# Optimization experiments

Hardware: AMD Instinct MI355X
Metric: run time of the kernel (lower is better)

The kernel has to match this reference:

```python
import jax, jax.numpy as jnp
import numpy as np

ROTARY_BASE = 10000
INFTY_APPROX = 1e30
B, T, M, H, D = 2, 2048, 2048, 16, 128


def rope(x):
    # x: [B, T, H, D]; half-split rotary encoding
    *_, length, _, width = x.shape
    half = width // 2
    positions = jnp.arange(length, dtype=jnp.float32)[None, :, None, None]      # [1,T,1,1]
    dims = jnp.arange(half, dtype=jnp.float32)
    ang_freqs = jnp.power(float(ROTARY_BASE), -dims / half)[None, None, None, :]  # [1,1,1,D/2]
    radians = positions * ang_freqs
    cos = jnp.cos(radians).astype(x.dtype)
    sin = jnp.sin(radians).astype(x.dtype)
    even, odd = x[..., :half], x[..., half:]
    r_even = even * cos - odd * sin
    r_odd = even * sin + odd * cos
    return jnp.concatenate([r_even, r_odd], axis=-1)


def setup_inputs() -> dict:
    key = jax.random.key(0)
    k0, k1, k2, k3, k4 = jax.random.split(key, 5)
    return {
        "x": jax.random.normal(k0, (B, T, M), dtype=jnp.float32),
        "w_aq": jax.random.normal(k1, (H, M, D), dtype=jnp.float32) * (M ** -0.5),
        "w_ak": jax.random.normal(k2, (H, M, D), dtype=jnp.float32) * (M ** -0.5),
        "w_av": jax.random.normal(k3, (H, M, D), dtype=jnp.float32) * (M ** -0.5),
        "w_ao": jax.random.normal(k4, (H, D, M), dtype=jnp.float32) * ((2 * 24 * M) ** -0.5),
    }


def reference(x, w_aq, w_ak, w_av, w_ao):
    q = jnp.einsum("btm,hmd->bthd", x, w_aq)
    k = jnp.einsum("btm,hmd->bthd", x, w_ak)
    v = jnp.einsum("btm,hmd->bthd", x, w_av)
    q = rope(q)
    k = rope(k)
    # muP attention scaling: 1/d_head (not 1/sqrt(d_head))
    mult = (1.0 / D) ** 0.5
    s = jnp.einsum("bihd,bjhd->bhij", mult * q, mult * k)  # [B,H,T,T]
    i = jnp.arange(T)[:, None]
    j = jnp.arange(T)[None, :]
    mask = (i < j)[None, None, :, :]  # mask future positions
    s = s - jnp.asarray(INFTY_APPROX, dtype=x.dtype) * mask
    p = jax.nn.softmax(s, axis=-1)
    o = jnp.einsum("bhij,bjhd->bihd", p, v)
    r = jnp.einsum("bihd,hdm->bim", o, w_ao)
    return r
```

## Files before the change

### kernel.cpp

```cpp
#include <hip/hip_runtime.h>

#define Bb 2
#define Tt 2048
#define Mm 2048
#define Hh 16
#define Dd 128

typedef __attribute__((ext_vector_type(8))) short bf16x8;
typedef __attribute__((ext_vector_type(4))) float f32x4;
typedef __attribute__((ext_vector_type(16))) float f32x16;

__device__ __forceinline__ unsigned short f2bf(float f) {
    unsigned int u = __builtin_bit_cast(unsigned int, f);
    u += 0x7FFFu + ((u >> 16) & 1u);
    return (unsigned short)(u >> 16);
}

__device__ __forceinline__ unsigned int cvt_pk_bf16(float lo, float hi) {
    unsigned int r;
    asm("v_cvt_pk_bf16_f32 %0, %1, %2" : "=v"(r) : "v"(lo), "v"(hi));
    return r;
}

__device__ __forceinline__ float fexp2(float x) { return __builtin_amdgcn_exp2f(x); }

__device__ __forceinline__ void gld16(const void* g, void* l) {
    __builtin_amdgcn_global_load_lds(
        (const __attribute__((address_space(1))) void*)g,
        (__attribute__((address_space(3))) void*)l, 16, 0, 0);
}


__global__ __launch_bounds__(256) void cvt_x2(const float* __restrict__ x,
                                              unsigned short* __restrict__ xb2) {
    const int blk = blockIdx.x;
    const int mt = blk >> 5, kt = blk & 31;
#pragma unroll
    for (int it = 0; it < 4; ++it) {
        int s = it * 256 + threadIdx.x;
        int row = ((s >> 6) & 3) * 32 + (s & 31);
        int k = (s >> 8) * 16 + ((s >> 5) & 1) * 8;
        const float* sp = x + ((long)(mt * 128 + row)) * 2048 + kt * 64 + k;
        float4 a = *(const float4*)sp;
        float4 b = *(const float4*)(sp + 4);
        uint4 pk;
        pk.x = (unsigned int)f2bf(a.x) | ((unsigned int)f2bf(a.y) << 16);
        pk.y = (unsigned int)f2bf(a.z) | ((unsigned int)f2bf(a.w) << 16);
        pk.z = (unsigned int)f2bf(b.x) | ((unsigned int)f2bf(b.y) << 16);
        pk.w = (unsigned int)f2bf(b.z) | ((unsigned int)f2bf(b.w) << 16);
        *(uint4*)(xb2 + (((long)(mt * 32 + kt)) * 1024 + s) * 8) = pk;
    }
}

__global__ __launch_bounds__(256) void w_qkv_tile(
    const float* __restrict__ wq, const float* __restrict__ wk, const float* __restrict__ wv,
    unsigned short* __restrict__ outBase) {
    __shared__ float tile[64][132];
    const int kt = blockIdx.x;
    const int zy = blockIdx.y;
    const int which = zy >> 4, head = zy & 15;
    const float* src = (which == 0 ? wq : which == 1 ? wk : wv) + (long)head * 2048 * 128;
    const int tid = threadIdx.x;
#pragma unroll
    for (int it = 0; it < 8; ++it) {
        int f = it * 256 + tid;
        int row = f >> 5, c4 = f & 31;
        float4 v = *(const float4*)(src + (long)(kt * 64 + row) * 128 + c4 * 4);
        tile[row][c4 * 4 + 0] = v.x;
        tile[row][c4 * 4 + 1] = v.y;
        tile[row][c4 * 4 + 2] = v.z;
        tile[row][c4 * 4 + 3] = v.w;
    }
    __syncthreads();
    unsigned short* outp = outBase + (((long)(which * 16 + head)) * 32 + kt) * 1024 * 8;
#pragma unroll
    for (int it = 0; it < 4; ++it) {
        int up = it * 256 + tid;
        int kk = up >> 8, nf = (up >> 6) & 3, l = up & 63;
        int il = l & 31, hl = l >> 5;
        int d = il + 64 * (nf & 1) + 32 * (nf >> 1);
        int kl = kk * 16 + hl * 8;
        uint4 pk;
        pk.x = (unsigned int)f2bf(tile[kl + 0][d]) | ((unsigned int)f2bf(tile[kl + 1][d]) << 16);
        pk.y = (unsigned int)f2bf(tile[kl + 2][d]) | ((unsigned int)f2bf(tile[kl + 3][d]) << 16);
        pk.z = (unsigned int)f2bf(tile[kl + 4][d]) | ((unsigned int)f2bf(tile[kl + 5][d]) << 16);
        pk.w = (unsigned int)f2bf(tile[kl + 6][d]) | ((unsigned int)f2bf(tile[kl + 7][d]) << 16);
        *(uint4*)(outp + (long)up * 8) = pk;
    }
}

__global__ __launch_bounds__(256) void transpose_cvt(const float* __restrict__ in,
                                                     unsigned short* __restrict__ out,
                                                     int rows, int cols,
                                                     long in_slab, long out_slab) {
    __shared__ float tile[32][33];
    const float* ip = in + (long)blockIdx.z * in_slab;
    unsigned short* op = out + (long)blockIdx.z * out_slab;
    int r0 = blockIdx.x * 32, c0 = blockIdx.y * 32;
    int tx = threadIdx.x & 31, ty = threadIdx.x >> 5;
#pragma unroll
    for (int j = 0; j < 32; j += 8)
        tile[ty + j][tx] = ip[(long)(r0 + ty + j) * cols + c0 + tx];
    __syncthreads();
#pragma unroll
    for (int j = 0; j < 32; j += 8)
        op[(long)(c0 + ty + j) * rows + r0 + tx] = f2bf(tile[tx][ty + j]);
}

__global__ __launch_bounds__(256) void rope_tab(float* __restrict__ cosT,
                                                float* __restrict__ sinT) {
    int idx = blockIdx.x * 256 + threadIdx.x;
    int t = idx >> 6, d = idx & 63;
    float freq = powf(10000.f, -(float)d / 64.f);
    float ang = (float)t * freq;
    sinT[idx] = sinf(ang);
    cosT[idx] = cosf(ang);
}

template <bool WIDE>
__device__ __forceinline__ void proj_sub(
    const unsigned short* __restrict__ xb2,
    const unsigned short* __restrict__ wT2,
    char* lds, int bm, int offc,
    unsigned short* __restrict__ qO, unsigned short* __restrict__ kO,
    unsigned short* __restrict__ vtO,
    const float* __restrict__ cosT, const float* __restrict__ sinT, int tid) {
    const int lane = tid & 63, wave = tid >> 6;
    const int il = lane & 31, hl = lane >> 5;
    const int wm = WIDE ? (wave >> 2) : (wave >> 1);
    const int wn = WIDE ? (wave & 3) : (wave & 1);
    const int hseg0 = offc >> 7;
    const int mode = offc >> 11;
    constexpr int MF = WIDE ? 4 : 2;

    f32x16 acc[MF][2];
#pragma unroll
    for (int a = 0; a < MF; ++a)
#pragma unroll
        for (int b2 = 0; b2 < 2; ++b2)
#pragma unroll
            for (int e = 0; e < 16; ++e) acc[a][b2][e] = 0.f;

    auto stage = [&](int buf, int t, int half) {
        const int kt = t >> 1, hf = t & 1;
        char* dst = lds + buf * 32768;
        if (WIDE) {
#pragma unroll
            for (int i = 0; i < 2; ++i) {
                int f = (half * 2 + i) * 512 + tid;
                if (f < 1024) {
                    int kk = f >> 9, rf = (f >> 6) & 7, l = f & 63;
                    int mt = 2 * bm + (rf >> 2), rb = rf & 3;
                    gld16(xb2 + (((long)(mt * 32 + kt)) * 1024 + (2 * hf + kk) * 256 + rb * 64 + l) * 8,
                          dst + f * 16);
                } else {
                    int g = f - 1024;
                    int kk = g >> 9, cf = (g >> 6) & 7, l = g & 63;
                    int hs = hseg0 + (cf >> 2), nf = cf & 3;
                    gld16(wT2 + (((long)(hs * 32 + kt)) * 1024 + (2 * hf + kk) * 256 + nf * 64 + l) * 8,
                          dst + 16384 + g * 16);
                }
            }
        } else {
            const int i0 = half ? 2 : 0, i1 = half ? 3 : 2;
            for (int i = i0; i < i1; ++i) {
                int f = i * 512 + tid;
                if (f < 1024) {
                    int kk = f >> 9, rf = (f >> 6) & 7, l = f & 63;
                    int mt = 2 * bm + (rf >> 2), rb = rf & 3;
                    gld16(xb2 + (((long)(mt * 32 + kt)) * 1024 + (2 * hf + kk) * 256 + rb * 64 + l) * 8,
                          dst + f * 16);
                } else {
                    int g = f - 1024;
                    int kk = g >> 8, nf = (g >> 6) & 3, l = g & 63;
                    gld16(wT2 + (((long)(hseg0 * 32 + kt)) * 1024 + (2 * hf + kk) * 256 + nf * 64 + l) * 8,
                          dst + 16384 + g * 16);
                }
            }
        }
    };

    stage(0, 0, 0); stage(0, 0, 1);
    stage(1, 1, 0); stage(1, 1, 1);

    int cur = 0;
    for (int t = 0; t < 64; ++t) {
        int pre = cur + 2; if (pre >= 3) pre -= 3;
        const char* bc = lds + cur * 32768;

        if (t + 2 < 64) {
            stage(pre, t + 2, 0);
            if (WIDE) asm volatile("s_waitcnt vmcnt(6)" ::: "memory");
            else      asm volatile("s_waitcnt vmcnt(5)" ::: "memory");
        } else if (t == 62) {
            if (WIDE) asm volatile("s_waitcnt vmcnt(4)" ::: "memory");
            else      asm volatile("s_waitcnt vmcnt(3)" ::: "memory");
        } else {
            asm volatile("s_waitcnt vmcnt(0)" ::: "memory");
        }
        asm volatile("s_barrier" ::: "memory");
        {
            bf16x8 af[MF], bf[2];
#pragma unroll
            for (int mf = 0; mf < MF; ++mf)
                af[mf] = *(const bf16x8*)(bc + ((wm * MF + mf) * 64 + lane) * 16);
#pragma unroll
            for (int nf = 0; nf < 2; ++nf)
                bf[nf] = *(const bf16x8*)(bc + 16384 + ((wn * 2 + nf) * 64 + lane) * 16);
            asm volatile("s_waitcnt lgkmcnt(0)" ::: "memory");
            __builtin_amdgcn_s_setprio(1);
#pragma unroll
            for (int mf = 0; mf < MF; ++mf)
#pragma unroll
                for (int nf = 0; nf < 2; ++nf)
                    acc[mf][nf] = __builtin_amdgcn_mfma_f32_32x32x16_bf16(af[mf], bf[nf], acc[mf][nf], 0, 0, 0);
            __builtin_amdgcn_s_setprio(0);
        }
        asm volatile("s_barrier" ::: "memory");

        if (t + 2 < 64) stage(pre, t + 2, 1);
        asm volatile("s_barrier" ::: "memory");
        {
            constexpr int BO = WIDE ? 512 : 256;
            bf16x8 af[MF], bf[2];
#pragma unroll
            for (int mf = 0; mf < MF; ++mf)
                af[mf] = *(const bf16x8*)(bc + (512 + (wm * MF + mf) * 64 + lane) * 16);
#pragma unroll
            for (int nf = 0; nf < 2; ++nf)
                bf[nf] = *(const bf16x8*)(bc + 16384 + (BO + (wn * 2 + nf) * 64 + lane) * 16);
            asm volatile("s_waitcnt lgkmcnt(0)" ::: "memory");
            __builtin_amdgcn_s_setprio(1);
#pragma unroll
            for (int mf = 0; mf < MF; ++mf)
#pragma unroll
                for (int nf = 0; nf < 2; ++nf)
                    acc[mf][nf] = __builtin_amdgcn_mfma_f32_32x32x16_bf16(af[mf], bf[nf], acc[mf][nf], 0, 0, 0);
            __builtin_amdgcn_s_setprio(0);
        }
        asm volatile("s_barrier" ::: "memory");
        cur = (cur == 2) ? 0 : cur + 1;
    }
    asm volatile("s_waitcnt vmcnt(0)" ::: "memory");
    __syncthreads();

    const int b = bm >> 3;
    const int t0 = (bm & 7) * 256;
    const int head_g = WIDE ? (hseg0 + (wn >> 1)) : hseg0;
    const int head_l = head_g & 15;
    const int opar = WIDE ? (wn & 1) : wn;
    constexpr int WMS = WIDE ? 128 : 64;

    if (mode < 2) {
        const float qs = (mode == 0) ? 0.011271055f : 1.0f;
        unsigned short* outp = (mode == 0) ? qO : kO;
        long hb = ((long)(b * Hh + head_l)) * Tt;
        int d_lo = il + 32 * opar;
#pragma unroll
        for (int mf = 0; mf < MF; ++mf)
#pragma unroll
            for (int reg = 0; reg < 16; ++reg) {
                int r = (reg & 3) + 8 * (reg >> 2) + 4 * hl;
                int tt = t0 + wm * WMS + mf * 32 + r;
                float c = cosT[tt * 64 + d_lo], s = sinT[tt * 64 + d_lo];
                float ev = acc[mf][0][reg], od = acc[mf][1][reg];
                long base = (hb + tt) * Dd;
                outp[base + d_lo]      = f2bf((ev * c - od * s) * qs);
                outp[base + d_lo + 64] = f2bf((ev * s + od * c) * qs);
            }
    } else {
        char* patch = lds + wave * 4096;
        long hdbase = ((long)(b * Hh + head_l)) * Dd * Tt;
#pragma unroll
        for (int mf = 0; mf < MF; ++mf) {
#pragma unroll
            for (int nf = 0; nf < 2; ++nf) {
                int dslot = nf * 32 + il;
                int swz = (dslot & 3) << 4;
#pragma unroll
                for (int qg = 0; qg < 4; ++qg) {
                    uint2 w;
                    w.x = cvt_pk_bf16(acc[mf][nf][qg * 4 + 0], acc[mf][nf][qg * 4 + 1]);
                    w.y = cvt_pk_bf16(acc[mf][nf][qg * 4 + 2], acc[mf][nf][qg * 4 + 3]);
                    *(uint2*)(patch + dslot * 64 + ((qg * 16 + hl * 8) ^ swz)) = w;
                }
            }
            __builtin_amdgcn_s_waitcnt(0);
#pragma unroll
            for (int p = 0; p < 4; ++p) {
                int dslot = p * 16 + (lane >> 2);
                int t8 = lane & 3;
                uint4 v = *(const uint4*)(patch + dslot * 64 + ((t8 * 16) ^ ((dslot & 3) << 4)));
                int o = opar * 2 + (dslot >> 5), il2 = dslot & 31;
                int dd = il2 + 32 * (o >> 1) + 64 * (o & 1);
                int tg = t0 + wm * WMS + mf * 32 + t8 * 8;
                *(uint4*)(vtO + hdbase + (long)dd * Tt + tg) = v;
            }
            __builtin_amdgcn_s_waitcnt(0);
        }
    }
}

__global__ __launch_bounds__(512, 2) void proj_gemm7(
    const unsigned short* __restrict__ xb2,
    const unsigned short* __restrict__ wT2,
    unsigned short* __restrict__ qO,
    unsigned short* __restrict__ kO,
    unsigned short* __restrict__ vtO,
    const float* __restrict__ cosT,
    const float* __restrict__ sinT) {
    __shared__ __align__(16) char lds[98304];
    const int bm = blockIdx.x;
    const int bc = blockIdx.y;
    const int s = bc * 384;
    const bool swap = ((s & 2047) == 1920);
    const int offw = swap ? s + 128 : s;
    const int offn = swap ? s : s + 256;
    const int tid = threadIdx.x;

    proj_sub<true>(xb2, wT2, lds, bm, offw, qO, kO, vtO, cosT, sinT, tid);
    __syncthreads();
    proj_sub<false>(xb2, wT2, lds, bm, offn, qO, kO, vtO, cosT, sinT, tid);
}

__global__ __launch_bounds__(256) void attn_kernel(
    const unsigned short* __restrict__ q,
    const unsigned short* __restrict__ k,
    const unsigned short* __restrict__ vt,
    unsigned short* __restrict__ o) {
    __shared__ __align__(16) unsigned short lds[32768];

    const int lid = (int)blockIdx.x;
    const int p = lid & 255;
    const int bh = p & 31;
    const int q0 = p >> 5;
    const int qb = (lid >> 8) ? (15 - q0) : q0;

    const int tid = threadIdx.x, lane = tid & 63, wave = tid >> 6;
    const int h = lane >> 5, iln = lane & 31;

    const unsigned short* qp = q + (long)bh * Tt * Dd;
    const unsigned short* kp = k + (long)bh * Tt * Dd;
    const unsigned short* vp = vt + (long)bh * Dd * Tt;

    const int i_g = qb * 128 + wave * 32 + iln;
    bf16x8 qf[8];
#pragma unroll
    for (int kk = 0; kk < 8; ++kk)
        qf[kk] = *(const bf16x8*)(qp + (long)i_g * Dd + kk * 16 + h * 8);

    f32x16 accO[4];
#pragma unroll
    for (int nb = 0; nb < 4; ++nb)
#pragma unroll
        for (int e = 0; e < 16; ++e) accO[nb][e] = 0.f;

    float m_r = -1e30f, l_r = 0.f;
    const int ntiles = 2 * qb + 2;

    auto stage = [&](int buf, int tix) {
        const int j0s = tix * 64;
#pragma unroll
        for (int it = 0; it < 4; ++it) {
            int f = it * 256 + tid;
            int rk = f >> 4, ck = f & 15;
            gld16(kp + ((long)(j0s + rk) * Dd + ((ck ^ (rk & 7)) << 3)),
                  (char*)lds + buf * 16384 + f * 16);
            int rv = f >> 3, cv = f & 7;
            gld16(vp + ((long)rv * Tt + j0s + ((cv ^ (rv & 7)) << 3)),
                  (char*)lds + 32768 + buf * 16384 + f * 16);
        }
    };

    stage(0, 0);

    for (int tix = 0; tix < ntiles; ++tix) {
        const int cur = tix & 1;
        const int j0 = tix * 64;
        if (tix + 1 < ntiles) {
            stage(cur ^ 1, tix + 1);
            asm volatile("s_waitcnt vmcnt(8)" ::: "memory");
        } else {
            asm volatile("s_waitcnt vmcnt(0)" ::: "memory");
        }
        __builtin_amdgcn_s_barrier();

        const char* Kb = (const char*)lds + cur * 16384;
        const char* Vb = (const char*)lds + 32768 + cur * 16384;

        f32x16 sacc[2];
#pragma unroll
        for (int mb = 0; mb < 2; ++mb)
#pragma unroll
            for (int e = 0; e < 16; ++e) sacc[mb][e] = 0.f;

        __builtin_amdgcn_s_setprio(1);
#pragma unroll
        for (int mb = 0; mb < 2; ++mb) {
            int row = mb * 32 + iln;
            const char* Kr = Kb + row * 256;
            int sw = row & 7;
#pragma unroll
            for (int kk = 0; kk < 8; ++kk) {
                bf16x8 kf = *(const bf16x8*)(Kr + 16 * ((kk * 2 + h) ^ sw));
                sacc[mb] = __builtin_amdgcn_mfma_f32_32x32x16_bf16(kf, qf[kk], sacc[mb], 0, 0, 0);
            }
        }
        __builtin_amdgcn_s_setprio(0);

        const bool domask = (j0 + 63 > qb * 128);
        if (domask) {
#pragma unroll
            for (int mb = 0; mb < 2; ++mb)
#pragma unroll
                for (int reg = 0; reg < 16; ++reg) {
                    int j = j0 + mb * 32 + (reg & 3) + 8 * (reg >> 2) + 4 * h;
                    if (j > i_g) sacc[mb][reg] = -1e30f;
                }
        }

        float red[16];
#pragma unroll
        for (int r = 0; r < 16; ++r) red[r] = fmaxf(sacc[0][r], sacc[1][r]);
#pragma unroll
        for (int s = 8; s >= 1; s >>= 1)
#pragma unroll
            for (int r = 0; r < s; ++r) red[r] = fmaxf(red[r], red[r + s]);
        float mx = fmaxf(red[0], __shfl_xor(red[0], 32, 64));

        if (__any(mx > m_r + 8.f)) {
            float mn = fmaxf(m_r, mx);
            float corr = fexp2(m_r - mn);
            m_r = mn;
            l_r *= corr;
#pragma unroll
            for (int reg = 0; reg < 16; ++reg) {
                int rrow = (reg & 3) + 8 * (reg >> 2) + 4 * h;
                float c = __shfl(corr, rrow, 64);
#pragma unroll
                for (int nb = 0; nb < 4; ++nb) accO[nb][reg] *= c;
            }
        }

        float pe[2][16];
#pragma unroll
        for (int mb = 0; mb < 2; ++mb)
#pragma unroll
            for (int r = 0; r < 16; ++r) pe[mb][r] = fexp2(sacc[mb][r] - m_r);
        float sr[16];
#pragma unroll
        for (int r = 0; r < 16; ++r) sr[r] = pe[0][r] + pe[1][r];
#pragma unroll
        for (int s = 8; s >= 1; s >>= 1)
#pragma unroll
            for (int r = 0; r < s; ++r) sr[r] += sr[r + s];
        l_r += sr[0] + __shfl_xor(sr[0], 32, 64);

        unsigned int pu[2][8];
#pragma unroll
        for (int mb = 0; mb < 2; ++mb)
#pragma unroll
            for (int t = 0; t < 8; ++t)
                pu[mb][t] = cvt_pk_bf16(pe[mb][2 * t], pe[mb][2 * t + 1]);

        unsigned int rv2[2][4];
#pragma unroll
        for (int mb = 0; mb < 2; ++mb)
#pragma unroll
            for (int u = 0; u < 4; ++u) {
                unsigned int sv = h ? pu[mb][(u & 1) + 4 * (u >> 1)]
                                    : pu[mb][2 + (u & 1) + 4 * (u >> 1)];
                rv2[mb][u] = __shfl_xor(sv, 32, 64);
            }

        __builtin_amdgcn_s_setprio(1);
#pragma unroll
        for (int kk2 = 0; kk2 < 4; ++kk2) {
            const int mb = kk2 >> 1, c2 = kk2 & 1;
            unsigned int w0 = h ? rv2[mb][2 * c2 + 0] : pu[mb][4 * c2 + 0];
            unsigned int w1 = h ? rv2[mb][2 * c2 + 1] : pu[mb][4 * c2 + 1];
            unsigned int w2 = h ? pu[mb][4 * c2 + 2] : rv2[mb][2 * c2 + 0];
            unsigned int w3 = h ? pu[mb][4 * c2 + 3] : rv2[mb][2 * c2 + 1];
            uint4 aw; aw.x = w0; aw.y = w1; aw.z = w2; aw.w = w3;
            bf16x8 af = __builtin_bit_cast(bf16x8, aw);
#pragma unroll
            for (int nb = 0; nb < 4; ++nb) {
                int dd = nb * 32 + iln;
                int byte = dd * 128 + 16 * ((kk2 * 2 + h) ^ (dd & 7));
                bf16x8 vf = *(const bf16x8*)(Vb + byte);
                accO[nb] = __builtin_amdgcn_mfma_f32_32x32x16_bf16(af, vf, accO[nb], 0, 0, 0);
            }
        }
        __builtin_amdgcn_s_setprio(0);

        asm volatile("" ::: "memory");
        __builtin_amdgcn_s_barrier();
    }

    const int b = bh >> 4, hh = bh & 15;
    float invl = 1.f / l_r;
#pragma unroll
    for (int reg = 0; reg < 16; ++reg) {
        int rrow = (reg & 3) + 8 * (reg >> 2) + 4 * h;
        float iv = __shfl(invl, rrow, 64);
        int t = qb * 128 + wave * 32 + rrow;
        long base = ((long)(b * Tt + t) * Hh + hh) * Dd;
#pragma unroll
        for (int nb = 0; nb < 4; ++nb)
            o[base + nb * 32 + iln] = f2bf(accO[nb][reg] * iv);
    }
}

__global__ __launch_bounds__(256) void out_gemm(
    const unsigned short* __restrict__ oIn,
    const unsigned short* __restrict__ woT,
    float* __restrict__ out) {
    __shared__ __align__(16) unsigned short smem[32768];
    const int bm = blockIdx.x, bn = blockIdx.y;
    const int tid = threadIdx.x;
    const int lane = tid & 63;
    const int wave = tid >> 6;
    const int g = lane >> 4;
    const int ln = lane & 15;

    const unsigned short* arow = oIn + (long)bm * 128 * Mm;
    const unsigned short* brow = woT + (long)bn * 128 * Mm;

    f32x4 acc[2][8];
#pragma unroll
    for (int a = 0; a < 2; ++a)
#pragma unroll
        for (int b2 = 0; b2 < 8; ++b2)
#pragma unroll
            for (int e = 0; e < 4; ++e) acc[a][b2][e] = 0.f;

    auto stage = [&](int buf, int kt) {
        const int k0 = kt * 64;
#pragma unroll
        for (int it = 0; it < 4; ++it) {
            int f = it * 256 + tid;
            int r = f >> 3, c = f & 7;
            long off = (long)r * Mm + k0 + ((c ^ (r & 7)) << 3);
            gld16(arow + off, (char*)smem + buf * 32768 + f * 16);
            gld16(brow + off, (char*)smem + buf * 32768 + 16384 + f * 16);
        }
    };

    stage(0, 0);

    for (int kt = 0; kt < Mm / 64; ++kt) {
        const int cur = kt & 1;
        if (kt + 1 < Mm / 64) {
            stage(cur ^ 1, kt + 1);
            asm volatile("s_waitcnt vmcnt(8)" ::: "memory");
        } else {
            asm volatile("s_waitcnt vmcnt(0)" ::: "memory");
        }
        __builtin_amdgcn_s_barrier();

        const char* Ab = (const char*)smem + cur * 32768;
        const char* Bv = Ab + 16384;
#pragma unroll
        for (int kc = 0; kc < 2; ++kc) {
            bf16x8 af[2];
#pragma unroll
            for (int rf = 0; rf < 2; ++rf) {
                int row = wave * 32 + rf * 16 + ln;
                int byte = (row * 128 + kc * 64 + g * 16) ^ ((row & 7) << 4);
                af[rf] = *(const bf16x8*)(Ab + byte);
            }
#pragma unroll
            for (int ni = 0; ni < 8; ++ni) {
                int row = ni * 16 + ln;
                int byte = (row * 128 + kc * 64 + g * 16) ^ ((row & 7) << 4);
                bf16x8 bfv = *(const bf16x8*)(Bv + byte);
#pragma unroll
                for (int rf = 0; rf < 2; ++rf)
                    acc[rf][ni] = __builtin_amdgcn_mfma_f32_16x16x32_bf16(af[rf], bfv, acc[rf][ni], 0, 0, 0);
            }
        }
        asm volatile("" ::: "memory");
        __builtin_amdgcn_s_barrier();
    }

#pragma unroll
    for (int rf = 0; rf < 2; ++rf)
#pragma unroll
        for (int reg = 0; reg < 4; ++reg) {
            long row = bm * 128 + wave * 32 + rf * 16 + g * 4 + reg;
#pragma unroll
            for (int ni = 0; ni < 8; ++ni)
                out[row * Mm + bn * 128 + ni * 16 + ln] = acc[rf][ni][reg];
        }
}


extern "C" void kernel_launch(void* const* d_in, const int* in_sizes, int n_in,
                              void* d_out, int out_size, void* d_ws, size_t ws_size,
                              hipStream_t stream) {
    const float* x    = (const float*)d_in[0];
    const float* w_aq = (const float*)d_in[1];
    const float* w_ak = (const float*)d_in[2];
    const float* w_av = (const float*)d_in[3];
    const float* w_ao = (const float*)d_in[4];
    float* out = (float*)d_out;

    char* ws = (char*)d_ws;
    const long SZ_BTM = 16777216;
    const long SZ_W   = 8388608;
    unsigned short* xb2 = (unsigned short*)(ws);
    unsigned short* qB  = (unsigned short*)(ws + SZ_BTM);
    unsigned short* kB  = (unsigned short*)(ws + 2 * SZ_BTM);
    unsigned short* vtB = (unsigned short*)(ws + 3 * SZ_BTM);
    unsigned short* oB  = (unsigned short*)(ws + 4 * SZ_BTM);
    unsigned short* wT2 = (unsigned short*)(ws + 5 * SZ_BTM);
    unsigned short* woT = (unsigned short*)(ws + 5 * SZ_BTM + 3 * SZ_W);
    float* cosT = (float*)(ws + 5 * SZ_BTM + 4 * SZ_W);
    float* sinT = (float*)(ws + 5 * SZ_BTM + 4 * SZ_W + 524288);

    cvt_x2<<<1024, 256, 0, stream>>>(x, xb2);
    w_qkv_tile<<<dim3(32, 48), 256, 0, stream>>>(w_aq, w_ak, w_av, wT2);
    transpose_cvt<<<dim3(64, 64, 1), 256, 0, stream>>>(w_ao, woT, 2048, 2048, 0, 0);
    rope_tab<<<512, 256, 0, stream>>>(cosT, sinT);

    proj_gemm7<<<dim3(16, 16), 512, 0, stream>>>(xb2, wT2, qB, kB, vtB, cosT, sinT);
    attn_kernel<<<dim3(512), 256, 0, stream>>>(qB, kB, vtB, oB);
    out_gemm<<<dim3(32, 16), 256, 0, stream>>>(oB, woT, out);
}
```

Before: 262.0 us.

## Register double-buffer LDS fragments in projection GEMM and cut a barrier in output GEMM

The projection GEMM main loop now stages a whole k-tile per step into a 3-deep LDS ring. It loads the next tile's fragments into a second register set while the MFMAs run on the current set, which cuts the barriers per iteration from four to one and hides LDS latency behind MFMA. The output GEMM now issues its next-tile global prefetch after a full vmcnt(0) wait and a barrier, and drops the trailing barrier. That saves one barrier per iteration, but it also removes the overlap of the global load with the wait. Register pressure grows from the doubled fragment arrays, which could hurt occupancy under the 512x2 launch bounds.

```diff
diff --git a/kernel.cpp b/kernel.cpp
--- a/kernel.cpp
+++ b/kernel.cpp
@@ -118,7 +118,7 @@
 }
 
 template <bool WIDE>
-__device__ __forceinline__ void proj_sub(
+__device__ __forceinline__ void proj_sub9(
     const unsigned short* __restrict__ xb2,
     const unsigned short* __restrict__ wT2,
     char* lds, int bm, int offc,
@@ -132,6 +132,8 @@
     const int hseg0 = offc >> 7;
     const int mode = offc >> 11;
     constexpr int MF = WIDE ? 4 : 2;
+    constexpr int NFR = WIDE ? 12 : 8;
+    constexpr int FS = WIDE ? 6 : 4;
 
     f32x16 acc[MF][2];
 #pragma unroll
@@ -141,108 +143,103 @@
 #pragma unroll
             for (int e = 0; e < 16; ++e) acc[a][b2][e] = 0.f;
 
-    auto stage = [&](int buf, int t, int half) {
-        const int kt = t >> 1, hf = t & 1;
-        char* dst = lds + buf * 32768;
+    auto stageTo = [&](int bufOff, int kt2) {
+        const int kt = kt2 >> 1, hf = kt2 & 1;
+        char* dst = lds + bufOff;
+#pragma unroll
+        for (int i = 0; i < 2; ++i) {
+            int f = i * 512 + tid;
+            int kk = f >> 9, rf = (f >> 6) & 7, l = f & 63;
+            int mt = 2 * bm + (rf >> 2), rb = rf & 3;
+            gld16(xb2 + (((long)(mt * 32 + kt)) * 1024 + (2 * hf + kk) * 256 + rb * 64 + l) * 8,
+                  dst + f * 16);
+        }
         if (WIDE) {
 #pragma unroll
             for (int i = 0; i < 2; ++i) {
-                int f = (half * 2 + i) * 512 + tid;
-                if (f < 1024) {
-                    int kk = f >> 9, rf = (f >> 6) & 7, l = f & 63;
-                    int mt = 2 * bm + (rf >> 2), rb = rf & 3;
-                    gld16(xb2 + (((long)(mt * 32 + kt)) * 1024 + (2 * hf + kk) * 256 + rb * 64 + l) * 8,
-                          dst + f * 16);
-                } else {
-                    int g = f - 1024;
-                    int kk = g >> 9, cf = (g >> 6) & 7, l = g & 63;
-                    int hs = hseg0 + (cf >> 2), nf = cf & 3;
-                    gld16(wT2 + (((long)(hs * 32 + kt)) * 1024 + (2 * hf + kk) * 256 + nf * 64 + l) * 8,
-                          dst + 16384 + g * 16);
-                }
+                int g = i * 512 + tid;
+                int kk = g >> 9, cf = (g >> 6) & 7, l = g & 63;
+                int hs = hseg0 + (cf >> 2), nf = cf & 3;
+                gld16(wT2 + (((long)(hs * 32 + kt)) * 1024 + (2 * hf + kk) * 256 + nf * 64 + l) * 8,
+                      dst + 16384 + g * 16);
             }
         } else {
-            const int i0 = half ? 2 : 0, i1 = half ? 3 : 2;
-            for (int i = i0; i < i1; ++i) {
-                int f = i * 512 + tid;
-                if (f < 1024) {
-                    int kk = f >> 9, rf = (f >> 6) & 7, l = f & 63;
-                    int mt = 2 * bm + (rf >> 2), rb = rf & 3;
-                    gld16(xb2 + (((long)(mt * 32 + kt)) * 1024 + (2 * hf + kk) * 256 + rb * 64 + l) * 8,
-                          dst + f * 16);
-                } else {
-                    int g = f - 1024;
-                    int kk = g >> 8, nf = (g >> 6) & 3, l = g & 63;
-                    gld16(wT2 + (((long)(hseg0 * 32 + kt)) * 1024 + (2 * hf + kk) * 256 + nf * 64 + l) * 8,
-                          dst + 16384 + g * 16);
-                }
-            }
+            int g = tid;
+            int kk = g >> 8, nf = (g >> 6) & 3, l = g & 63;
+            gld16(wT2 + (((long)(hseg0 * 32 + kt)) * 1024 + (2 * hf + kk) * 256 + nf * 64 + l) * 8,
+                  dst + 16384 + g * 16);
         }
     };
 
-    stage(0, 0, 0); stage(0, 0, 1);
-    stage(1, 1, 0); stage(1, 1, 1);
-
-    int cur = 0;
-    for (int t = 0; t < 64; ++t) {
-        int pre = cur + 2; if (pre >= 3) pre -= 3;
-        const char* bc = lds + cur * 32768;
-
-        if (t + 2 < 64) {
-            stage(pre, t + 2, 0);
-            if (WIDE) asm volatile("s_waitcnt vmcnt(6)" ::: "memory");
-            else      asm volatile("s_waitcnt vmcnt(5)" ::: "memory");
-        } else if (t == 62) {
-            if (WIDE) asm volatile("s_waitcnt vmcnt(4)" ::: "memory");
-            else      asm volatile("s_waitcnt vmcnt(3)" ::: "memory");
-        } else {
-            asm volatile("s_waitcnt vmcnt(0)" ::: "memory");
-        }
-        asm volatile("s_barrier" ::: "memory");
+    auto prefetch = [&](bf16x8 (&fr)[NFR], int bufOff) {
+        const char* bc = lds + bufOff;
+#pragma unroll
+        for (int kk2 = 0; kk2 < 2; ++kk2) {
+#pragma unroll
+            for (int mf = 0; mf < MF; ++mf)
+                fr[kk2 * FS + mf] = *(const bf16x8*)(bc + (kk2 * 512 + (wm * MF + mf) * 64 + lane) * 16);
+#pragma unroll
+            for (int nf = 0; nf < 2; ++nf)
+                fr[kk2 * FS + MF + nf] = *(const bf16x8*)(bc + 16384 +
+                    ((WIDE ? kk2 * 512 : kk2 * 256) + (wn * 2 + nf) * 64 + lane) * 16);
+        }
+    };
+
+    auto domfma = [&](bf16x8 (&fr)[NFR]) {
+        __builtin_amdgcn_s_setprio(1);
+#pragma unroll
+        for (int kk2 = 0; kk2 < 2; ++kk2)
+#pragma unroll
+            for (int mf = 0; mf < MF; ++mf)
+#pragma unroll
+                for (int nf = 0; nf < 2; ++nf)
+                    acc[mf][nf] = __builtin_amdgcn_mfma_f32_32x32x16_bf16(
+                        fr[kk2 * FS + mf], fr[kk2 * FS + MF + nf], acc[mf][nf], 0, 0, 0);
+        __builtin_amdgcn_s_setprio(0);
+    };
+
+    bf16x8 fA[NFR], fB[NFR];
+
+    stageTo(0, 0);
+    stageTo(32768, 1);
+    if (WIDE) asm volatile("s_waitcnt vmcnt(4)" ::: "memory");
+    else      asm volatile("s_waitcnt vmcnt(3)" ::: "memory");
+    __builtin_amdgcn_s_barrier();
+    prefetch(fA, 0);
+
+    int curOff = 0;
+    for (int p = 0; p < 31; ++p) {
         {
-            bf16x8 af[MF], bf[2];
-#pragma unroll
-            for (int mf = 0; mf < MF; ++mf)
-                af[mf] = *(const bf16x8*)(bc + ((wm * MF + mf) * 64 + lane) * 16);
-#pragma unroll
-            for (int nf = 0; nf < 2; ++nf)
-                bf[nf] = *(const bf16x8*)(bc + 16384 + ((wn * 2 + nf) * 64 + lane) * 16);
-            asm volatile("s_waitcnt lgkmcnt(0)" ::: "memory");
-            __builtin_amdgcn_s_setprio(1);
-#pragma unroll
-            for (int mf = 0; mf < MF; ++mf)
-#pragma unroll
-                for (int nf = 0; nf < 2; ++nf)
-                    acc[mf][nf] = __builtin_amdgcn_mfma_f32_32x32x16_bf16(af[mf], bf[nf], acc[mf][nf], 0, 0, 0);
-            __builtin_amdgcn_s_setprio(0);
-        }
-        asm volatile("s_barrier" ::: "memory");
-
-        if (t + 2 < 64) stage(pre, t + 2, 1);
-        asm volatile("s_barrier" ::: "memory");
+            int preOff = curOff + 65536; if (preOff >= 98304) preOff -= 98304;
+            stageTo(preOff, 2 * p + 2);
+            if (WIDE) asm volatile("s_waitcnt vmcnt(4) lgkmcnt(0)" ::: "memory");
+            else      asm volatile("s_waitcnt vmcnt(3) lgkmcnt(0)" ::: "memory");
+            __builtin_amdgcn_s_barrier();
+            int nxtOff = curOff + 32768; if (nxtOff >= 98304) nxtOff -= 98304;
+            prefetch(fB, nxtOff);
+            domfma(fA);
+            curOff = nxtOff;
+        }
         {
-            constexpr int BO = WIDE ? 512 : 256;
-            bf16x8 af[MF], bf[2];
-#pragma unroll
-            for (int mf = 0; mf < MF; ++mf)
-                af[mf] = *(const bf16x8*)(bc + (512 + (wm * MF + mf) * 64 + lane) * 16);
-#pragma unroll
-            for (int nf = 0; nf < 2; ++nf)
-                bf[nf] = *(const bf16x8*)(bc + 16384 + (BO + (wn * 2 + nf) * 64 + lane) * 16);
-            asm volatile("s_waitcnt lgkmcnt(0)" ::: "memory");
-            __builtin_amdgcn_s_setprio(1);
-#pragma unroll
-            for (int mf = 0; mf < MF; ++mf)
-#pragma unroll
-                for (int nf = 0; nf < 2; ++nf)
-                    acc[mf][nf] = __builtin_amdgcn_mfma_f32_32x32x16_bf16(af[mf], bf[nf], acc[mf][nf], 0, 0, 0);
-            __builtin_amdgcn_s_setprio(0);
-        }
-        asm volatile("s_barrier" ::: "memory");
-        cur = (cur == 2) ? 0 : cur + 1;
-    }
-    asm volatile("s_waitcnt vmcnt(0)" ::: "memory");
-    __syncthreads();
+            int preOff = curOff + 65536; if (preOff >= 98304) preOff -= 98304;
+            stageTo(preOff, 2 * p + 3);
+            if (WIDE) asm volatile("s_waitcnt vmcnt(4) lgkmcnt(0)" ::: "memory");
+            else      asm volatile("s_waitcnt vmcnt(3) lgkmcnt(0)" ::: "memory");
+            __builtin_amdgcn_s_barrier();
+            int nxtOff = curOff + 32768; if (nxtOff >= 98304) nxtOff -= 98304;
+            prefetch(fA, nxtOff);
+            domfma(fB);
+            curOff = nxtOff;
+        }
+    }
+    asm volatile("s_waitcnt vmcnt(0) lgkmcnt(0)" ::: "memory");
+    __builtin_amdgcn_s_barrier();
+    {
+        int nxtOff = curOff + 32768; if (nxtOff >= 98304) nxtOff -= 98304;
+        prefetch(fB, nxtOff);
+        domfma(fA);
+    }
+    domfma(fB);
 
     const int b = bm >> 3;
     const int t0 = (bm & 7) * 256;
@@ -269,6 +266,7 @@
                 outp[base + d_lo + 64] = f2bf((ev * s + od * c) * qs);
             }
     } else {
+        __syncthreads();
         char* patch = lds + wave * 4096;
         long hdbase = ((long)(b * Hh + head_l)) * Dd * Tt;
 #pragma unroll
@@ -287,8 +285,8 @@
             }
             __builtin_amdgcn_s_waitcnt(0);
 #pragma unroll
-            for (int p = 0; p < 4; ++p) {
-                int dslot = p * 16 + (lane >> 2);
+            for (int p2 = 0; p2 < 4; ++p2) {
+                int dslot = p2 * 16 + (lane >> 2);
                 int t8 = lane & 3;
                 uint4 v = *(const uint4*)(patch + dslot * 64 + ((t8 * 16) ^ ((dslot & 3) << 4)));
                 int o = opar * 2 + (dslot >> 5), il2 = dslot & 31;
@@ -301,7 +299,7 @@
     }
 }
 
-__global__ __launch_bounds__(512, 2) void proj_gemm7(
+__global__ __launch_bounds__(512, 2) void proj_gemm9(
     const unsigned short* __restrict__ xb2,
     const unsigned short* __restrict__ wT2,
     unsigned short* __restrict__ qO,
@@ -318,9 +316,9 @@
     const int offn = swap ? s : s + 256;
     const int tid = threadIdx.x;
 
-    proj_sub<true>(xb2, wT2, lds, bm, offw, qO, kO, vtO, cosT, sinT, tid);
+    proj_sub9<true>(xb2, wT2, lds, bm, offw, qO, kO, vtO, cosT, sinT, tid);
     __syncthreads();
-    proj_sub<false>(xb2, wT2, lds, bm, offn, qO, kO, vtO, cosT, sinT, tid);
+    proj_sub9<false>(xb2, wT2, lds, bm, offn, qO, kO, vtO, cosT, sinT, tid);
 }
 
 __global__ __launch_bounds__(256) void attn_kernel(
@@ -550,13 +548,9 @@
 
     for (int kt = 0; kt < Mm / 64; ++kt) {
         const int cur = kt & 1;
-        if (kt + 1 < Mm / 64) {
-            stage(cur ^ 1, kt + 1);
-            asm volatile("s_waitcnt vmcnt(8)" ::: "memory");
-        } else {
-            asm volatile("s_waitcnt vmcnt(0)" ::: "memory");
-        }
+        asm volatile("s_waitcnt vmcnt(0)" ::: "memory");
         __builtin_amdgcn_s_barrier();
+        if (kt + 1 < Mm / 64) stage(cur ^ 1, kt + 1);
 
         const char* Ab = (const char*)smem + cur * 32768;
         const char* Bv = Ab + 16384;
@@ -580,7 +574,6 @@
             }
         }
         asm volatile("" ::: "memory");
-        __builtin_amdgcn_s_barrier();
     }
 
 #pragma unroll
@@ -623,7 +616,7 @@
     transpose_cvt<<<dim3(64, 64, 1), 256, 0, stream>>>(w_ao, woT, 2048, 2048, 0, 0);
     rope_tab<<<512, 256, 0, stream>>>(cosT, sinT);
 
-    proj_gemm7<<<dim3(16, 16), 512, 0, stream>>>(xb2, wT2, qB, kB, vtB, cosT, sinT);
+    proj_gemm9<<<dim3(16, 16), 512, 0, stream>>>(xb2, wT2, qB, kB, vtB, cosT, sinT);
     attn_kernel<<<dim3(512), 256, 0, stream>>>(qB, kB, vtB, oB);
     out_gemm<<<dim3(32, 16), 256, 0, stream>>>(oB, woT, out);
 }
```

Measured after the change: 251.4 us. -4.0%, faster.
